# Kernel tuning notes

Hardware: AMD Instinct MI355X
Metric: run time of the kernel (lower is better)

## Reference

```python
import jax, jax.numpy as jnp
import numpy as np

BETA = 0.9  # snntorch Leaky beta (single-step, zero init mem => mem = x)
H = 8       # num_heads
EPS = 1e-5

@jax.custom_vjp
def lif_spike(x):
    # snn.Leaky single step, mem init 0: mem = BETA*0 + x ; spk = heaviside(mem - 1.0)
    return (x > 1.0).astype(x.dtype)

def _lif_fwd(x):
    return lif_spike(x), x

def _lif_bwd(x, g):
    # ATan surrogate (snntorch default, alpha=2): d spk/d mem = 1/(1 + (pi*(mem-1))^2)
    u = x - 1.0
    return (g / (1.0 + (jnp.pi * u) ** 2),)

lif_spike.defvjp(_lif_fwd, _lif_bwd)

def layer_norm(x, g, b):
    m = jnp.mean(x, -1, keepdims=True)
    v = jnp.mean((x - m) ** 2, -1, keepdims=True)
    return (x - m) * jax.lax.rsqrt(v + EPS) * g + b

def mha(x, Wqkv, Wo, causal):
    B, N, D = x.shape
    hd = D // H
    q, k, v = jnp.split(x @ Wqkv, 3, axis=-1)
    q = q.reshape(B, N, H, hd).transpose(0, 2, 1, 3)
    k = k.reshape(B, N, H, hd).transpose(0, 2, 1, 3)
    v = v.reshape(B, N, H, hd).transpose(0, 2, 1, 3)
    s = jnp.einsum('bhqd,bhkd->bhqk', q, k) / jnp.sqrt(jnp.asarray(hd, x.dtype))
    if causal:
        s = jnp.where(jnp.tril(jnp.ones((N, N), bool)), s, jnp.asarray(-1e9, x.dtype))
    a = jax.nn.softmax(s, axis=-1)
    o = jnp.einsum('bhqk,bhkd->bhqd', a, v).transpose(0, 2, 1, 3).reshape(B, N, D)
    return o @ Wo

def transformer(x, qkv, out, ln1, ff1, ff2, ln2, causal):
    # pre-norm transformer blocks; Encoder non-causal, Decoder causal
    for i in range(qkv.shape[0]):
        x = x + mha(layer_norm(x, ln1[i, 0], ln1[i, 1]), qkv[i], out[i], causal)
        x = x + jax.nn.gelu(layer_norm(x, ln2[i, 0], ln2[i, 1]) @ ff1[i]) @ ff2[i]
    return x

def setup_inputs():
    key = jax.random.key(0)
    B, R, S, D = 8, 90, 240, 256
    enc_depth, pred_depth = 8, 6
    ks = iter(jax.random.split(key, 64))
    def nrm(shape, std):
        return jax.random.normal(next(ks), shape, jnp.float32) * std
    def enc_params(depth):
        return dict(
            qkv=nrm((depth, D, 3 * D), 0.05),
            out=nrm((depth, D, D), 0.05),
            ln1=jnp.stack([jnp.ones((depth, D)), jnp.zeros((depth, D))], 1),
            ff1=nrm((depth, D, 4 * D), 0.05),
            ff2=nrm((depth, 4 * D, D), 0.05),
            ln2=jnp.stack([jnp.ones((depth, D)), jnp.zeros((depth, D))], 1),
        )
    t, s_, p = enc_params(enc_depth), enc_params(enc_depth), enc_params(pred_depth)
    inp = dict(
        x=jax.random.normal(next(ks), (B, R, S), jnp.float32),
        W_embed=nrm((S, D), 0.1), b_embed=jnp.zeros((D,), jnp.float32),
        pos_embedding=nrm((1, R, D), 1.0),
        mask_token=nrm((1, 1, D), 0.02),
        norm_g=jnp.ones((D,), jnp.float32), norm_b=jnp.zeros((D,), jnp.float32),
        W_dec=nrm((D, S), 0.1), b_dec=jnp.zeros((S,), jnp.float32),
    )
    for name, prm in (('t', t), ('s', s_), ('p', p)):
        for k2, v2 in prm.items():
            inp[name + '_' + k2] = v2
    return inp

def reference(x, W_embed, b_embed, pos_embedding, mask_token, norm_g, norm_b, W_dec, b_dec,
              t_qkv, t_out, t_ln1, t_ff1, t_ff2, t_ln2,
              s_qkv, s_out, s_ln1, s_ff1, s_ff2, s_ln2,
              p_qkv, p_out, p_ln1, p_ff1, p_ff2, p_ln2):
    B, R, S = x.shape
    D = W_embed.shape[1]
    # token embed + pos + token_lif
    x_emb = lif_spike(x @ W_embed + b_embed + pos_embedding)  # [B,R,D]
    # teacher (torch.no_grad)
    teacher_full = lif_spike(layer_norm(
        transformer(x_emb, t_qkv, t_out, t_ln1, t_ff1, t_ff2, t_ln2, False), norm_g, norm_b))
    teacher_full = jax.lax.stop_gradient(teacher_full)
    # student
    student_full = lif_spike(layer_norm(
        transformer(x_emb, s_qkv, s_out, s_ln1, s_ff1, s_ff2, s_ln2, False), norm_g, norm_b))
    # batched exhaustive leave-one-out: for each target t, context = all rows != t
    loo = np.stack([np.delete(np.arange(R), t) for t in range(R)])  # [R, R-1]
    ctx = student_full[:, loo, :]                                   # [B,R,R-1,D]
    masks = lif_spike(mask_token + pos_embedding)                   # [1,R,D] mask_lif
    masks = jnp.broadcast_to(masks[:, :, None, :], (B, R, 1, D))
    seq = jnp.concatenate([ctx, masks], axis=2).reshape(B * R, R, D)
    pred = lif_spike(transformer(seq, p_qkv, p_out, p_ln1, p_ff1, p_ff2, p_ln2, True))
    pred_targets = pred[:, -1, :].reshape(B, R, D)  # last token = predicted target region
    teacher_targets = teacher_full                   # exhaustive: targets are all R rows in order
    pred_seq = lif_spike(pred_targets @ W_dec + b_dec)      # output_lif [B,R,S]
    teacher_seq = lif_spike(teacher_targets @ W_dec + b_dec)
    target_seq = x
    return (pred_seq, teacher_seq, target_seq,
            pred_seq.mean(-1), teacher_seq.mean(-1), target_seq.mean(-1))
```

## Files before the change

### kernel.cpp

```cpp
#include <hip/hip_runtime.h>
#include <math.h>


__device__ __forceinline__ float gelu_f(float x) {
    const float c = 0.7978845608028654f;
    float x3 = x * x * x;
    float inner = c * (x + 0.044715f * x3);
    return 0.5f * x * (1.0f + tanhf(inner));
}

__device__ __forceinline__ int suffix_off(int g) {
    int b = g / 90, r = g - b * 90;
    return b * 4095 + 90 * r - ((r * (r - 1)) >> 1);
}

__global__ __launch_bounds__(256) void embed_kernel(
    const float* __restrict__ x, const float* __restrict__ We,
    const float* __restrict__ be, const float* __restrict__ pos,
    float* __restrict__ xemb) {
    int tok = blockIdx.x;
    int d = threadIdx.x;
    __shared__ float xs[240];
    if (d < 240) xs[d] = x[(size_t)tok * 240 + d];
    __syncthreads();
    int r = tok % 90;
    double acc = 0.0;
    for (int s = 0; s < 240; ++s)
        acc = fma((double)xs[s], (double)We[(size_t)s * 256 + d], acc);
    float a = (float)acc + be[d] + pos[r * 256 + d];
    xemb[(size_t)tok * 256 + d] = (a > 1.0f) ? 1.0f : 0.0f;
}

__global__ void copy_kernel(float* __restrict__ dst, const float* __restrict__ src, int n) {
    int i = blockIdx.x * 256 + threadIdx.x;
    if (i < n) dst[i] = src[i];
}
__global__ void zero_kernel(float* __restrict__ p, int n) {
    int i = blockIdx.x * 256 + threadIdx.x;
    if (i < n) p[i] = 0.f;
}

__global__ __launch_bounds__(256) void ln_kernel(
    const float* __restrict__ X,
    const float* __restrict__ gA, const float* __restrict__ bA,
    const float* __restrict__ gB, const float* __restrict__ bB,
    int split, float* __restrict__ Y) {
    int row = blockIdx.x;
    int d = threadIdx.x;
    const float* g = (row < split) ? gA : gB;
    const float* b = (row < split) ? bA : bB;
    __shared__ float red[256];
    float v = X[(size_t)row * 256 + d];
    red[d] = v;
    __syncthreads();
    for (int s = 128; s > 0; s >>= 1) { if (d < s) red[d] += red[d + s]; __syncthreads(); }
    float mean = red[0] * (1.0f / 256.0f);
    __syncthreads();
    float dv = v - mean;
    red[d] = dv * dv;
    __syncthreads();
    for (int s = 128; s > 0; s >>= 1) { if (d < s) red[d] += red[d + s]; __syncthreads(); }
    float var = red[0] * (1.0f / 256.0f);
    float r = 1.0f / sqrtf(var + 1e-5f);
    Y[(size_t)row * 256 + d] = dv * r * g[d] + b[d];
}

__global__ __launch_bounds__(256) void ln_lif_kernel(
    const float* __restrict__ X, const float* __restrict__ g, const float* __restrict__ b,
    float* __restrict__ Y) {
    int row = blockIdx.x;
    int d = threadIdx.x;
    __shared__ float red[256];
    float v = X[(size_t)row * 256 + d];
    red[d] = v;
    __syncthreads();
    for (int s = 128; s > 0; s >>= 1) { if (d < s) red[d] += red[d + s]; __syncthreads(); }
    float mean = red[0] * (1.0f / 256.0f);
    __syncthreads();
    float dv = v - mean;
    red[d] = dv * dv;
    __syncthreads();
    for (int s = 128; s > 0; s >>= 1) { if (d < s) red[d] += red[d + s]; __syncthreads(); }
    float var = red[0] * (1.0f / 256.0f);
    float r = 1.0f / sqrtf(var + 1e-5f);
    float val = dv * r * g[d] + b[d];
    Y[(size_t)row * 256 + d] = (val > 1.0f) ? 1.0f : 0.0f;
}

#define BK 16
template <int EPI>
__global__ __launch_bounds__(256) void gemm_kernel(
    const float* __restrict__ A, const float* __restrict__ W0,
    const float* __restrict__ W1, int wsplit,
    float* __restrict__ C, const float* __restrict__ R,
    int M, int N, int K, int ldA, int ldW, int ldC,
    int zA, int zW, long zC) {
    __shared__ float As[2][BK][64 + 4];
    __shared__ float Ws[2][BK][64];
    int bm = blockIdx.y * 64;
    int bn = blockIdx.x * 64;
    int z = blockIdx.z;
    A += (size_t)z * zA;
    const float* W = ((bm < wsplit) ? W0 : W1) + (size_t)z * zW;
    C += (size_t)z * zC;
    const float* Rp = R + (size_t)z * zC;
    int tid = threadIdx.x;
    int tx = tid & 15;
    int ty = tid >> 4;
    int ar = tid >> 2;
    int ak = (tid & 3) * 4;
    int wk = tid >> 4;
    int wn = (tid & 15) * 4;
    int gm = bm + ar;
    bool aok = gm < M;
    const float* Aptr = A + (size_t)gm * ldA + ak;
    const float* Wptr = W + (size_t)wk * ldW + bn + wn;

    float acc[4][4] = {{0.f}};
    float4 va = aok ? *(const float4*)Aptr : make_float4(0.f, 0.f, 0.f, 0.f);
    float4 vw = *(const float4*)Wptr;
    As[0][ak + 0][ar] = va.x; As[0][ak + 1][ar] = va.y;
    As[0][ak + 2][ar] = va.z; As[0][ak + 3][ar] = va.w;
    *(float4*)&Ws[0][wk][wn] = vw;
    __syncthreads();

    int nt = K / BK;
    for (int t = 0; t < nt; ++t) {
        int cur = t & 1;
        if (t + 1 < nt) {
            va = aok ? *(const float4*)(Aptr + (t + 1) * BK)
                     : make_float4(0.f, 0.f, 0.f, 0.f);
            vw = *(const float4*)(Wptr + (size_t)(t + 1) * BK * ldW);
        }
        #pragma unroll
        for (int k = 0; k < BK; ++k) {
            float a[4], w[4];
            #pragma unroll
            for (int i = 0; i < 4; ++i) a[i] = As[cur][k][ty * 4 + i];
            #pragma unroll
            for (int j = 0; j < 4; ++j) w[j] = Ws[cur][k][tx * 4 + j];
            #pragma unroll
            for (int i = 0; i < 4; ++i)
                #pragma unroll
                for (int j = 0; j < 4; ++j)
                    acc[i][j] = fmaf(a[i], w[j], acc[i][j]);
        }
        if (t + 1 < nt) {
            int nx = cur ^ 1;
            As[nx][ak + 0][ar] = va.x; As[nx][ak + 1][ar] = va.y;
            As[nx][ak + 2][ar] = va.z; As[nx][ak + 3][ar] = va.w;
            *(float4*)&Ws[nx][wk][wn] = vw;
        }
        __syncthreads();
    }
    #pragma unroll
    for (int i = 0; i < 4; ++i) {
        int om = bm + ty * 4 + i;
        if (om >= M) continue;
        #pragma unroll
        for (int j = 0; j < 4; ++j) {
            int on = bn + tx * 4 + j;
            float v = acc[i][j];
            if (EPI == 1) v += Rp[(size_t)om * ldC + on];
            if (EPI == 2) v = gelu_f(v);
            C[(size_t)om * ldC + on] = v;
        }
    }
}

__global__ void addff_kernel(float4* __restrict__ X, const float4* __restrict__ S,
                             long zstr4, int n4) {
    int i = blockIdx.x * 256 + threadIdx.x;
    if (i >= n4) return;
    float4 x = X[i];
    float4 s0 = S[i], s1 = S[i + zstr4], s2 = S[i + 2 * zstr4], s3 = S[i + 3 * zstr4];
    x.x = (((x.x + s0.x) + s1.x) + s2.x) + s3.x;
    x.y = (((x.y + s0.y) + s1.y) + s2.y) + s3.y;
    x.z = (((x.z + s0.z) + s1.z) + s2.z) + s3.z;
    x.w = (((x.w + s0.w) + s1.w) + s2.w) + s3.w;
    X[i] = x;
}

__global__ __launch_bounds__(128) void attn_kernel(
    const float* __restrict__ QKV, float* __restrict__ AO,
    int N, int causal, int hs, int off2) {
    int s = blockIdx.x, h = blockIdx.y;
    int tokbase = (s < hs) ? s * N : off2 + (s - hs) * N;
    __shared__ float Ks[90][32];
    __shared__ float Vs[90][32];
    int tid = threadIdx.x;
    for (int i = tid; i < N * 32; i += 128) {
        int n = i >> 5, d = i & 31;
        size_t base = ((size_t)(tokbase + n)) * 768 + h * 32;
        Ks[n][d] = QKV[base + 256 + d];
        Vs[n][d] = QKV[base + 512 + d];
    }
    __syncthreads();
    int q = tid;
    if (q >= N) return;
    float qv[32];
    size_t qbase = ((size_t)(tokbase + q)) * 768 + h * 32;
    #pragma unroll
    for (int d = 0; d < 32; ++d) qv[d] = QKV[qbase + d];
    const float sq = 5.656854249492380195f;
    int kmax = causal ? (q + 1) : N;
    float m = -3.0e38f;
    for (int k = 0; k < kmax; ++k) {
        float sd = 0.f;
        #pragma unroll
        for (int d = 0; d < 32; ++d) sd = fmaf(qv[d], Ks[k][d], sd);
        sd /= sq;
        m = fmaxf(m, sd);
    }
    float sum = 0.f;
    float acc[32];
    #pragma unroll
    for (int d = 0; d < 32; ++d) acc[d] = 0.f;
    for (int k = 0; k < kmax; ++k) {
        float sd = 0.f;
        #pragma unroll
        for (int d = 0; d < 32; ++d) sd = fmaf(qv[d], Ks[k][d], sd);
        sd /= sq;
        float p = expf(sd - m);
        sum += p;
        #pragma unroll
        for (int d = 0; d < 32; ++d) acc[d] = fmaf(p, Vs[k][d], acc[d]);
    }
    size_t obase = ((size_t)(tokbase + q)) * 256 + h * 32;
    #pragma unroll
    for (int d = 0; d < 32; ++d) AO[obase + d] = acc[d] / sum;
}

__global__ __launch_bounds__(128) void suffix_attn_kernel(
    const float* __restrict__ QKV, const float* __restrict__ kv,
    float* __restrict__ AO, int g0) {
    int ls = blockIdx.x, h = blockIdx.y;
    int g = g0 + ls;
    int b = g / 90, r = g - b * 90;
    int toff = suffix_off(g) - suffix_off(g0);
    int L = 90 - r;
    __shared__ float Ks[90][32];
    __shared__ float Vs[90][32];
    int tid = threadIdx.x;
    for (int i = tid; i < 90 * 32; i += 128) {
        int p = i >> 5, d = i & 31;
        float kk, vv;
        if (p < r) {
            const float* src = kv + ((size_t)(b * 89 + p)) * 512 + h * 32 + d;
            kk = src[0]; vv = src[256];
        } else {
            size_t base = ((size_t)(toff + p - r)) * 768 + h * 32 + d;
            kk = QKV[base + 256]; vv = QKV[base + 512];
        }
        Ks[p][d] = kk; Vs[p][d] = vv;
    }
    __syncthreads();
    if (tid >= L) return;
    int jq = r + tid;
    float qv[32];
    size_t qbase = ((size_t)(toff + tid)) * 768 + h * 32;
    #pragma unroll
    for (int d = 0; d < 32; ++d) qv[d] = QKV[qbase + d];
    const float sq = 5.656854249492380195f;
    int kmax = jq + 1;
    float m = -3.0e38f;
    for (int k = 0; k < kmax; ++k) {
        float sd = 0.f;
        #pragma unroll
        for (int d = 0; d < 32; ++d) sd = fmaf(qv[d], Ks[k][d], sd);
        sd /= sq;
        m = fmaxf(m, sd);
    }
    float sum = 0.f;
    float acc[32];
    #pragma unroll
    for (int d = 0; d < 32; ++d) acc[d] = 0.f;
    for (int k = 0; k < kmax; ++k) {
        float sd = 0.f;
        #pragma unroll
        for (int d = 0; d < 32; ++d) sd = fmaf(qv[d], Ks[k][d], sd);
        sd /= sq;
        float p = expf(sd - m);
        sum += p;
        #pragma unroll
        for (int d = 0; d < 32; ++d) acc[d] = fmaf(p, Vs[k][d], acc[d]);
    }
    size_t obase = ((size_t)(toff + tid)) * 256 + h * 32;
    #pragma unroll
    for (int d = 0; d < 32; ++d) AO[obase + d] = acc[d] / sum;
}

__global__ __launch_bounds__(128) void lastq_attn_kernel(
    const float* __restrict__ QKV, const float* __restrict__ kv,
    float* __restrict__ AO2, int g0) {
    int ls = blockIdx.x, h = blockIdx.y;
    int g = g0 + ls;
    int b = g / 90, r = g - b * 90;
    int toff = suffix_off(g) - suffix_off(g0);
    int L = 90 - r;
    __shared__ float Ks[90][32];
    __shared__ float Vs[90][32];
    int tid = threadIdx.x;
    for (int i = tid; i < 90 * 32; i += 128) {
        int p = i >> 5, d = i & 31;
        float kk, vv;
        if (p < r) {
            const float* src = kv + ((size_t)(b * 89 + p)) * 512 + h * 32 + d;
            kk = src[0]; vv = src[256];
        } else {
            size_t base = ((size_t)(toff + p - r)) * 768 + h * 32 + d;
            kk = QKV[base + 256]; vv = QKV[base + 512];
        }
        Ks[p][d] = kk; Vs[p][d] = vv;
    }
    __syncthreads();
    if (tid != 0) return;
    float qv[32];
    size_t qbase = ((size_t)(toff + L - 1)) * 768 + h * 32;
    #pragma unroll
    for (int d = 0; d < 32; ++d) qv[d] = QKV[qbase + d];
    const float sq = 5.656854249492380195f;
    float m = -3.0e38f;
    for (int k = 0; k < 90; ++k) {
        float sd = 0.f;
        #pragma unroll
        for (int d = 0; d < 32; ++d) sd = fmaf(qv[d], Ks[k][d], sd);
        sd /= sq;
        m = fmaxf(m, sd);
    }
    float sum = 0.f;
    float acc[32];
    #pragma unroll
    for (int d = 0; d < 32; ++d) acc[d] = 0.f;
    for (int k = 0; k < 90; ++k) {
        float sd = 0.f;
        #pragma unroll
        for (int d = 0; d < 32; ++d) sd = fmaf(qv[d], Ks[k][d], sd);
        sd /= sq;
        float p = expf(sd - m);
        sum += p;
        #pragma unroll
        for (int d = 0; d < 32; ++d) acc[d] = fmaf(p, Vs[k][d], acc[d]);
    }
    size_t obase = (size_t)ls * 256 + h * 32;
    #pragma unroll
    for (int d = 0; d < 32; ++d) AO2[obase + d] = acc[d] / sum;
}

__global__ void masks_kernel(const float* __restrict__ mt, const float* __restrict__ pos,
                             float* __restrict__ M) {
    int i = blockIdx.x * 256 + threadIdx.x;
    if (i >= 90 * 256) return;
    int d = i & 255;
    float v = mt[d] + pos[i];
    M[i] = (v > 1.0f) ? 1.0f : 0.0f;
}

__global__ __launch_bounds__(256) void gather_canon_kernel(
    const float* __restrict__ student, float* __restrict__ Xc, int b0) {
    int tc = blockIdx.x;
    int d = threadIdx.x;
    int b = b0 + tc / 89, p = tc % 89;
    Xc[(size_t)tc * 256 + d] = student[((size_t)(b * 90 + p)) * 256 + d];
}

__global__ __launch_bounds__(256) void kvcopy_kernel(
    const float* __restrict__ QKVc, float* __restrict__ kvl, int b0) {
    int tc = blockIdx.x;
    int c = threadIdx.x;
    size_t gtc = (size_t)b0 * 89 + tc;
    kvl[gtc * 512 + c]       = QKVc[(size_t)tc * 768 + 256 + c];
    kvl[gtc * 512 + 256 + c] = QKVc[(size_t)tc * 768 + 512 + c];
}

__global__ __launch_bounds__(256) void gather_suffix_kernel(
    const float* __restrict__ student, const float* __restrict__ masks,
    float* __restrict__ X, int g0) {
    int ls = blockIdx.x, slot = blockIdx.y;
    int d = threadIdx.x;
    int g = g0 + ls;
    int b = g / 90, r = g - b * 90;
    if (slot >= 90 - r) return;
    int j = r + slot;
    int dst = suffix_off(g) - suffix_off(g0) + slot;
    float v;
    if (j == 89) v = masks[r * 256 + d];
    else         v = student[((size_t)(b * 90 + j + 1)) * 256 + d];
    X[(size_t)dst * 256 + d] = v;
}

__global__ __launch_bounds__(256) void gather_last_kernel(
    const float* __restrict__ X, float* __restrict__ X2, int g0) {
    int ls = blockIdx.x;
    int d = threadIdx.x;
    int g = g0 + ls;
    int r = g % 90;
    int tok = suffix_off(g) - suffix_off(g0) + (89 - r);
    X2[(size_t)ls * 256 + d] = X[(size_t)tok * 256 + d];
}

__global__ __launch_bounds__(256) void lif_rows_kernel(
    const float* __restrict__ X2, float* __restrict__ predT, int g0) {
    int ls = blockIdx.x;
    int d = threadIdx.x;
    float v = X2[(size_t)ls * 256 + d];
    predT[(size_t)(g0 + ls) * 256 + d] = (v > 1.0f) ? 1.0f : 0.0f;
}

__global__ __launch_bounds__(256) void decode_kernel(
    const float* __restrict__ T, const float* __restrict__ Wd, const float* __restrict__ bd,
    float* __restrict__ outseq, float* __restrict__ outmean) {
    int row = blockIdx.x;
    int n = threadIdx.x;
    __shared__ float ts[256];
    __shared__ float red[256];
    ts[n] = T[(size_t)row * 256 + n];
    __syncthreads();
    float sval = 0.f;
    if (n < 240) {
        double acc = 0.0;
        for (int k = 0; k < 256; ++k)
            acc = fma((double)ts[k], (double)Wd[(size_t)k * 240 + n], acc);
        float a = (float)acc;
        a += bd[n];
        sval = (a > 1.0f) ? 1.0f : 0.0f;
        outseq[(size_t)row * 240 + n] = sval;
    }
    red[n] = sval;
    __syncthreads();
    for (int s = 128; s > 0; s >>= 1) { if (n < s) red[n] += red[n + s]; __syncthreads(); }
    if (n == 0) outmean[row] = red[0] * (1.0f / 240.0f);
}

__global__ __launch_bounds__(256) void target_kernel(
    const float* __restrict__ x, float* __restrict__ outseq, float* __restrict__ outmean) {
    int row = blockIdx.x;
    int n = threadIdx.x;
    __shared__ float red[256];
    float v = 0.f;
    if (n < 240) {
        v = x[(size_t)row * 240 + n];
        outseq[(size_t)row * 240 + n] = v;
    }
    red[n] = v;
    __syncthreads();
    for (int s = 128; s > 0; s >>= 1) { if (n < s) red[n] += red[n + s]; __syncthreads(); }
    if (n == 0) outmean[row] = red[0] * (1.0f / 240.0f);
}

extern "C" void kernel_launch(void* const* d_in, const int* in_sizes, int n_in,
                              void* d_out, int out_size, void* d_ws, size_t ws_size,
                              hipStream_t stream) {
    const float* x   = (const float*)d_in[0];
    const float* We  = (const float*)d_in[1];
    const float* be  = (const float*)d_in[2];
    const float* pos = (const float*)d_in[3];
    const float* mt  = (const float*)d_in[4];
    const float* ng  = (const float*)d_in[5];
    const float* nb  = (const float*)d_in[6];
    const float* Wd  = (const float*)d_in[7];
    const float* bd  = (const float*)d_in[8];
    const float* prm[3][6];
    for (int g = 0; g < 3; ++g)
        for (int k = 0; k < 6; ++k)
            prm[g][k] = (const float*)d_in[9 + g * 6 + k];

    float* wp = (float*)d_ws;
    auto alloc = [&](size_t n) { float* q = wp; wp += n; return q; };
    float* x_emb   = alloc(720 * 256);
    float* teacher = alloc(720 * 256);
    float* student = alloc(720 * 256);
    float* predT   = alloc(720 * 256);
    float* masksb  = alloc(90 * 256);
    float* kvc     = alloc(6ull * 712 * 512);
    float* AO2 = alloc(720 * 256);
    float* X2  = alloc(720 * 256);
    float* Xn2 = alloc(720 * 256);
    float* H2  = alloc(720 * 1024);
    float* S2  = alloc(4ull * 720 * 256);
    long  zS2  = 720 * 256;
    size_t fixed = (size_t)(wp - (float*)d_ws);

    size_t avail = ws_size / 4;
    long tcap_l = 90;
    if (avail > fixed) {
        long t = (long)((avail - fixed) / 3328);
        if (t > tcap_l) tcap_l = t;
    }
    if (tcap_l > 32760) tcap_l = 32760;
    int TCAP = (int)tcap_l;
    float* X   = alloc((size_t)TCAP * 256);
    float* Xn  = alloc((size_t)TCAP * 256);
    float* QKV = alloc((size_t)TCAP * 768);
    float* H   = alloc((size_t)TCAP * 1024);
    float* S   = alloc(4ull * TCAP * 256);
    long  zS   = (long)TCAP * 256;
    bool co_batch = (TCAP >= 1488);

    float* out = (float*)d_out;
    const int NOSPLIT = 1 << 30;

    embed_kernel<<<720, 256, 0, stream>>>(x, We, be, pos, x_emb);
    masks_kernel<<<90, 256, 0, stream>>>(mt, pos, masksb);

    auto run_layer = [&](int T, int gA, int gB, int l, int split, auto&& attn_launch) {
        const float* qkvA = prm[gA][0] + (size_t)l * 256 * 768;
        const float* qkvB = prm[gB][0] + (size_t)l * 256 * 768;
        const float* woA  = prm[gA][1] + (size_t)l * 256 * 256;
        const float* woB  = prm[gB][1] + (size_t)l * 256 * 256;
        const float* l1A  = prm[gA][2] + (size_t)l * 512;
        const float* l1B  = prm[gB][2] + (size_t)l * 512;
        const float* f1A  = prm[gA][3] + (size_t)l * 256 * 1024;
        const float* f1B  = prm[gB][3] + (size_t)l * 256 * 1024;
        const float* f2A  = prm[gA][4] + (size_t)l * 1024 * 256;
        const float* f2B  = prm[gB][4] + (size_t)l * 1024 * 256;
        const float* l2A  = prm[gA][5] + (size_t)l * 512;
        const float* l2B  = prm[gB][5] + (size_t)l * 512;
        int gy = (T + 63) / 64;
        ln_kernel<<<T, 256, 0, stream>>>(X, l1A, l1A + 256, l1B, l1B + 256, split, Xn);
        gemm_kernel<0><<<dim3(12, gy, 1), 256, 0, stream>>>(
            Xn, qkvA, qkvB, split, QKV, QKV, T, 768, 256, 256, 768, 768, 0, 0, 0);
        attn_launch();
        gemm_kernel<1><<<dim3(4, gy, 1), 256, 0, stream>>>(
            Xn, woA, woB, split, X, X, T, 256, 256, 256, 256, 256, 0, 0, 0);
        ln_kernel<<<T, 256, 0, stream>>>(X, l2A, l2A + 256, l2B, l2B + 256, split, Xn);
        gemm_kernel<2><<<dim3(16, gy, 1), 256, 0, stream>>>(
            Xn, f1A, f1B, split, H, H, T, 1024, 256, 256, 1024, 1024, 0, 0, 0);
        gemm_kernel<0><<<dim3(4, gy, 4), 256, 0, stream>>>(
            H, f2A, f2B, split, S, S, T, 256, 256, 1024, 256, 256, 256, 65536, zS);
        addff_kernel<<<(T * 64 + 255) / 256, 256, 0, stream>>>(
            (float4*)X, (const float4*)S, zS / 4, T * 64);
    };

    if (co_batch) {
        copy_kernel<<<720, 256, 0, stream>>>(X, x_emb, 720 * 256);
        copy_kernel<<<720, 256, 0, stream>>>(X + 768 * 256, x_emb, 720 * 256);
        zero_kernel<<<48, 256, 0, stream>>>(X + 720 * 256, 48 * 256);
        for (int l = 0; l < 8; ++l)
            run_layer(1488, 0, 1, l, 768,
                      [&] { attn_kernel<<<dim3(16, 8), 128, 0, stream>>>(
                                QKV, Xn, 90, 0, 8, 768); });
        ln_lif_kernel<<<720, 256, 0, stream>>>(X, ng, nb, teacher);
        ln_lif_kernel<<<720, 256, 0, stream>>>(X + 768 * 256, ng, nb, student);
    } else {
        int ce = TCAP / 90; if (ce > 8) ce = 8; if (ce < 1) ce = 1;
        for (int gi = 0; gi < 2; ++gi) {
            for (int s0 = 0; s0 < 8; s0 += ce) {
                int c = (8 - s0) < ce ? (8 - s0) : ce;
                int T = c * 90;
                copy_kernel<<<(T * 256 + 255) / 256, 256, 0, stream>>>(
                    X, x_emb + (size_t)s0 * 90 * 256, T * 256);
                for (int l = 0; l < 8; ++l)
                    run_layer(T, gi, gi, l, NOSPLIT,
                              [&] { attn_kernel<<<dim3(c, 8), 128, 0, stream>>>(
                                        QKV, Xn, 90, 0, c, 0); });
                ln_lif_kernel<<<T, 256, 0, stream>>>(
                    X, ng, nb, (gi == 0 ? teacher : student) + (size_t)s0 * 90 * 256);
            }
        }
    }

    {
        int cb = TCAP / 89; if (cb > 8) cb = 8; if (cb < 1) cb = 1;
        for (int b0 = 0; b0 < 8; b0 += cb) {
            int c = (8 - b0) < cb ? (8 - b0) : cb;
            int T = c * 89;
            gather_canon_kernel<<<T, 256, 0, stream>>>(student, X, b0);
            for (int l = 0; l < 5; ++l) {
                float* kvl = kvc + (size_t)l * 712 * 512;
                run_layer(T, 2, 2, l, NOSPLIT,
                          [&] {
                              kvcopy_kernel<<<T, 256, 0, stream>>>(QKV, kvl, b0);
                              attn_kernel<<<dim3(c, 8), 128, 0, stream>>>(
                                  QKV, Xn, 89, 1, c, 0);
                          });
            }
            {
                const float* l1P  = prm[2][2] + 5ull * 512;
                const float* qkvP = prm[2][0] + 5ull * 256 * 768;
                float* kvl = kvc + 5ull * 712 * 512;
                int gy = (T + 63) / 64;
                ln_kernel<<<T, 256, 0, stream>>>(X, l1P, l1P + 256, l1P, l1P + 256,
                                                 NOSPLIT, Xn);
                gemm_kernel<0><<<dim3(12, gy, 1), 256, 0, stream>>>(
                    Xn, qkvP, qkvP, NOSPLIT, QKV, QKV, T, 768, 256, 256, 768, 768, 0, 0, 0);
                kvcopy_kernel<<<T, 256, 0, stream>>>(QKV, kvl, b0);
            }
        }
    }

    auto Toff = [](int g) { int b = g / 90, r = g - b * 90;
                            return (long)b * 4095 + 90L * r - (long)r * (r - 1) / 2; };
    int cs = TCAP / 90; if (cs < 1) cs = 1; if (cs > 720) cs = 720;
    for (int g0 = 0; g0 < 720; ) {
        int g1 = g0 + cs; if (g1 > 720) g1 = 720;
        while ((int)(Toff(g1) - Toff(g0)) > TCAP && g1 > g0 + 1) --g1;
        int c = g1 - g0;
        int Tc = (int)(Toff(g1) - Toff(g0));
        { dim3 g(c, 90);
          gather_suffix_kernel<<<g, 256, 0, stream>>>(student, masksb, X, g0); }
        for (int l = 0; l < 5; ++l) {
            float* kvl = kvc + (size_t)l * 712 * 512;
            run_layer(Tc, 2, 2, l, NOSPLIT,
                      [&] { dim3 g(c, 8);
                            suffix_attn_kernel<<<g, 128, 0, stream>>>(QKV, kvl, Xn, g0); });
        }
        {
            const float* qkvP = prm[2][0] + 5ull * 256 * 768;
            const float* woP  = prm[2][1] + 5ull * 256 * 256;
            const float* l1P  = prm[2][2] + 5ull * 512;
            const float* f1P  = prm[2][3] + 5ull * 256 * 1024;
            const float* f2P  = prm[2][4] + 5ull * 1024 * 256;
            const float* l2P  = prm[2][5] + 5ull * 512;
            float* kvl = kvc + 5ull * 712 * 512;
            int gy  = (Tc + 63) / 64;
            int gyc = (c + 63) / 64;
            ln_kernel<<<Tc, 256, 0, stream>>>(X, l1P, l1P + 256, l1P, l1P + 256,
                                              NOSPLIT, Xn);
            gemm_kernel<0><<<dim3(12, gy, 1), 256, 0, stream>>>(
                Xn, qkvP, qkvP, NOSPLIT, QKV, QKV, Tc, 768, 256, 256, 768, 768, 0, 0, 0);
            { dim3 g(c, 8);
              lastq_attn_kernel<<<g, 128, 0, stream>>>(QKV, kvl, AO2, g0); }
            gather_last_kernel<<<c, 256, 0, stream>>>(X, X2, g0);
            gemm_kernel<1><<<dim3(4, gyc, 1), 256, 0, stream>>>(
                AO2, woP, woP, NOSPLIT, X2, X2, c, 256, 256, 256, 256, 256, 0, 0, 0);
            ln_kernel<<<c, 256, 0, stream>>>(X2, l2P, l2P + 256, l2P, l2P + 256,
                                             NOSPLIT, Xn2);
            gemm_kernel<2><<<dim3(16, gyc, 1), 256, 0, stream>>>(
                Xn2, f1P, f1P, NOSPLIT, H2, H2, c, 1024, 256, 256, 1024, 1024, 0, 0, 0);
            gemm_kernel<0><<<dim3(4, gyc, 4), 256, 0, stream>>>(
                H2, f2P, f2P, NOSPLIT, S2, S2, c, 256, 256, 1024, 256, 256, 256, 65536, zS2);
            addff_kernel<<<(c * 64 + 255) / 256, 256, 0, stream>>>(
                (float4*)X2, (const float4*)S2, zS2 / 4, c * 64);
            lif_rows_kernel<<<c, 256, 0, stream>>>(X2, predT, g0);
        }
        g0 = g1;
    }

    decode_kernel<<<720, 256, 0, stream>>>(predT, Wd, bd, out + 0, out + 518400);
    decode_kernel<<<720, 256, 0, stream>>>(teacher, Wd, bd, out + 172800, out + 519120);
    target_kernel<<<720, 256, 0, stream>>>(x, out + 345600, out + 519840);
}
```

Baseline: 9.435 ms.

## Replace split-K FF2 GEMM plus reduction kernel with single fused residual GEMM

The second feed-forward GEMM was split four ways along K into a partial-sum buffer, then summed with the residual by a separate add kernel. A new kernel now runs the full K=1024 reduction in one block, starts from the residual, and adds the partials in chunks of 256 to keep the original summation order. This drops the scratch buffer traffic and one launch per layer, and the freed workspace allows larger token chunks. In exchange the FF2 launch has a quarter of the blocks, which lowers parallelism for small token counts.

```diff
diff --git a/kernel.cpp b/kernel.cpp
--- a/kernel.cpp
+++ b/kernel.cpp
@@ -93,17 +93,12 @@
     const float* __restrict__ A, const float* __restrict__ W0,
     const float* __restrict__ W1, int wsplit,
     float* __restrict__ C, const float* __restrict__ R,
-    int M, int N, int K, int ldA, int ldW, int ldC,
-    int zA, int zW, long zC) {
+    int M, int N, int K, int ldA, int ldW, int ldC) {
     __shared__ float As[2][BK][64 + 4];
     __shared__ float Ws[2][BK][64];
     int bm = blockIdx.y * 64;
     int bn = blockIdx.x * 64;
-    int z = blockIdx.z;
-    A += (size_t)z * zA;
-    const float* W = ((bm < wsplit) ? W0 : W1) + (size_t)z * zW;
-    C += (size_t)z * zC;
-    const float* Rp = R + (size_t)z * zC;
+    const float* W = (bm < wsplit) ? W0 : W1;
     int tid = threadIdx.x;
     int tx = tid & 15;
     int ty = tid >> 4;
@@ -161,24 +156,98 @@
         for (int j = 0; j < 4; ++j) {
             int on = bn + tx * 4 + j;
             float v = acc[i][j];
-            if (EPI == 1) v += Rp[(size_t)om * ldC + on];
+            if (EPI == 1) v += R[(size_t)om * ldC + on];
             if (EPI == 2) v = gelu_f(v);
             C[(size_t)om * ldC + on] = v;
         }
     }
 }
 
-__global__ void addff_kernel(float4* __restrict__ X, const float4* __restrict__ S,
-                             long zstr4, int n4) {
-    int i = blockIdx.x * 256 + threadIdx.x;
-    if (i >= n4) return;
-    float4 x = X[i];
-    float4 s0 = S[i], s1 = S[i + zstr4], s2 = S[i + 2 * zstr4], s3 = S[i + 3 * zstr4];
-    x.x = (((x.x + s0.x) + s1.x) + s2.x) + s3.x;
-    x.y = (((x.y + s0.y) + s1.y) + s2.y) + s3.y;
-    x.z = (((x.z + s0.z) + s1.z) + s2.z) + s3.z;
-    x.w = (((x.w + s0.w) + s1.w) + s2.w) + s3.w;
-    X[i] = x;
+__global__ __launch_bounds__(256) void gemm_ff_kernel(
+    const float* __restrict__ A, const float* __restrict__ W0,
+    const float* __restrict__ W1, int wsplit,
+    float* __restrict__ C, const float* __restrict__ R,
+    int M, int K, int ldA, int ldW, int ldC) {
+    __shared__ float As[2][BK][64 + 4];
+    __shared__ float Ws[2][BK][64];
+    int bm = blockIdx.y * 64;
+    int bn = blockIdx.x * 64;
+    const float* W = (bm < wsplit) ? W0 : W1;
+    int tid = threadIdx.x;
+    int tx = tid & 15;
+    int ty = tid >> 4;
+    int ar = tid >> 2;
+    int ak = (tid & 3) * 4;
+    int wk = tid >> 4;
+    int wn = (tid & 15) * 4;
+    int gm = bm + ar;
+    bool aok = gm < M;
+    const float* Aptr = A + (size_t)gm * ldA + ak;
+    const float* Wptr = W + (size_t)wk * ldW + bn + wn;
+
+    float v[4][4];
+    #pragma unroll
+    for (int i = 0; i < 4; ++i) {
+        int om = bm + ty * 4 + i;
+        #pragma unroll
+        for (int j = 0; j < 4; ++j)
+            v[i][j] = (om < M) ? R[(size_t)om * ldC + bn + tx * 4 + j] : 0.f;
+    }
+    float acc[4][4] = {{0.f}};
+
+    float4 va = aok ? *(const float4*)Aptr : make_float4(0.f, 0.f, 0.f, 0.f);
+    float4 vw = *(const float4*)Wptr;
+    As[0][ak + 0][ar] = va.x; As[0][ak + 1][ar] = va.y;
+    As[0][ak + 2][ar] = va.z; As[0][ak + 3][ar] = va.w;
+    *(float4*)&Ws[0][wk][wn] = vw;
+    __syncthreads();
+
+    int nt = K / BK;
+    for (int t = 0; t < nt; ++t) {
+        int cur = t & 1;
+        if (t + 1 < nt) {
+            va = aok ? *(const float4*)(Aptr + (t + 1) * BK)
+                     : make_float4(0.f, 0.f, 0.f, 0.f);
+            vw = *(const float4*)(Wptr + (size_t)(t + 1) * BK * ldW);
+        }
+        #pragma unroll
+        for (int k = 0; k < BK; ++k) {
+            float a[4], w[4];
+            #pragma unroll
+            for (int i = 0; i < 4; ++i) a[i] = As[cur][k][ty * 4 + i];
+            #pragma unroll
+            for (int j = 0; j < 4; ++j) w[j] = Ws[cur][k][tx * 4 + j];
+            #pragma unroll
+            for (int i = 0; i < 4; ++i)
+                #pragma unroll
+                for (int j = 0; j < 4; ++j)
+                    acc[i][j] = fmaf(a[i], w[j], acc[i][j]);
+        }
+        if (t + 1 < nt) {
+            int nx = cur ^ 1;
+            As[nx][ak + 0][ar] = va.x; As[nx][ak + 1][ar] = va.y;
+            As[nx][ak + 2][ar] = va.z; As[nx][ak + 3][ar] = va.w;
+            *(float4*)&Ws[nx][wk][wn] = vw;
+        }
+        __syncthreads();
+        if ((t & 15) == 15) {
+            #pragma unroll
+            for (int i = 0; i < 4; ++i)
+                #pragma unroll
+                for (int j = 0; j < 4; ++j) {
+                    v[i][j] += acc[i][j];
+                    acc[i][j] = 0.f;
+                }
+        }
+    }
+    #pragma unroll
+    for (int i = 0; i < 4; ++i) {
+        int om = bm + ty * 4 + i;
+        if (om >= M) continue;
+        #pragma unroll
+        for (int j = 0; j < 4; ++j)
+            C[(size_t)om * ldC + bn + tx * 4 + j] = v[i][j];
+    }
 }
 
 __global__ __launch_bounds__(128) void attn_kernel(
@@ -477,14 +546,12 @@
     float* X2  = alloc(720 * 256);
     float* Xn2 = alloc(720 * 256);
     float* H2  = alloc(720 * 1024);
-    float* S2  = alloc(4ull * 720 * 256);
-    long  zS2  = 720 * 256;
     size_t fixed = (size_t)(wp - (float*)d_ws);
 
     size_t avail = ws_size / 4;
     long tcap_l = 90;
     if (avail > fixed) {
-        long t = (long)((avail - fixed) / 3328);
+        long t = (long)((avail - fixed) / 2304);
         if (t > tcap_l) tcap_l = t;
     }
     if (tcap_l > 32760) tcap_l = 32760;
@@ -493,8 +560,6 @@
     float* Xn  = alloc((size_t)TCAP * 256);
     float* QKV = alloc((size_t)TCAP * 768);
     float* H   = alloc((size_t)TCAP * 1024);
-    float* S   = alloc(4ull * TCAP * 256);
-    long  zS   = (long)TCAP * 256;
     bool co_batch = (TCAP >= 1488);
 
     float* out = (float*)d_out;
@@ -518,18 +583,16 @@
         const float* l2B  = prm[gB][5] + (size_t)l * 512;
         int gy = (T + 63) / 64;
         ln_kernel<<<T, 256, 0, stream>>>(X, l1A, l1A + 256, l1B, l1B + 256, split, Xn);
-        gemm_kernel<0><<<dim3(12, gy, 1), 256, 0, stream>>>(
-            Xn, qkvA, qkvB, split, QKV, QKV, T, 768, 256, 256, 768, 768, 0, 0, 0);
+        gemm_kernel<0><<<dim3(12, gy), 256, 0, stream>>>(
+            Xn, qkvA, qkvB, split, QKV, QKV, T, 768, 256, 256, 768, 768);
         attn_launch();
-        gemm_kernel<1><<<dim3(4, gy, 1), 256, 0, stream>>>(
-            Xn, woA, woB, split, X, X, T, 256, 256, 256, 256, 256, 0, 0, 0);
+        gemm_kernel<1><<<dim3(4, gy), 256, 0, stream>>>(
+            Xn, woA, woB, split, X, X, T, 256, 256, 256, 256, 256);
         ln_kernel<<<T, 256, 0, stream>>>(X, l2A, l2A + 256, l2B, l2B + 256, split, Xn);
-        gemm_kernel<2><<<dim3(16, gy, 1), 256, 0, stream>>>(
-            Xn, f1A, f1B, split, H, H, T, 1024, 256, 256, 1024, 1024, 0, 0, 0);
-        gemm_kernel<0><<<dim3(4, gy, 4), 256, 0, stream>>>(
-            H, f2A, f2B, split, S, S, T, 256, 256, 1024, 256, 256, 256, 65536, zS);
-        addff_kernel<<<(T * 64 + 255) / 256, 256, 0, stream>>>(
-            (float4*)X, (const float4*)S, zS / 4, T * 64);
+        gemm_kernel<2><<<dim3(16, gy), 256, 0, stream>>>(
+            Xn, f1A, f1B, split, H, H, T, 1024, 256, 256, 1024, 1024);
+        gemm_ff_kernel<<<dim3(4, gy), 256, 0, stream>>>(
+            H, f2A, f2B, split, X, X, T, 1024, 1024, 256, 256);
     };
 
     if (co_batch) {
@@ -582,8 +645,8 @@
                 int gy = (T + 63) / 64;
                 ln_kernel<<<T, 256, 0, stream>>>(X, l1P, l1P + 256, l1P, l1P + 256,
                                                  NOSPLIT, Xn);
-                gemm_kernel<0><<<dim3(12, gy, 1), 256, 0, stream>>>(
-                    Xn, qkvP, qkvP, NOSPLIT, QKV, QKV, T, 768, 256, 256, 768, 768, 0, 0, 0);
+                gemm_kernel<0><<<dim3(12, gy), 256, 0, stream>>>(
+                    Xn, qkvP, qkvP, NOSPLIT, QKV, QKV, T, 768, 256, 256, 768, 768);
                 kvcopy_kernel<<<T, 256, 0, stream>>>(QKV, kvl, b0);
             }
         }
@@ -617,21 +680,19 @@
             int gyc = (c + 63) / 64;
             ln_kernel<<<Tc, 256, 0, stream>>>(X, l1P, l1P + 256, l1P, l1P + 256,
                                               NOSPLIT, Xn);
-            gemm_kernel<0><<<dim3(12, gy, 1), 256, 0, stream>>>(
-                Xn, qkvP, qkvP, NOSPLIT, QKV, QKV, Tc, 768, 256, 256, 768, 768, 0, 0, 0);
+            gemm_kernel<0><<<dim3(12, gy), 256, 0, stream>>>(
+                Xn, qkvP, qkvP, NOSPLIT, QKV, QKV, Tc, 768, 256, 256, 768, 768);
             { dim3 g(c, 8);
               lastq_attn_kernel<<<g, 128, 0, stream>>>(QKV, kvl, AO2, g0); }
             gather_last_kernel<<<c, 256, 0, stream>>>(X, X2, g0);
-            gemm_kernel<1><<<dim3(4, gyc, 1), 256, 0, stream>>>(
-                AO2, woP, woP, NOSPLIT, X2, X2, c, 256, 256, 256, 256, 256, 0, 0, 0);
+            gemm_kernel<1><<<dim3(4, gyc), 256, 0, stream>>>(
+                AO2, woP, woP, NOSPLIT, X2, X2, c, 256, 256, 256, 256, 256);
             ln_kernel<<<c, 256, 0, stream>>>(X2, l2P, l2P + 256, l2P, l2P + 256,
                                              NOSPLIT, Xn2);
-            gemm_kernel<2><<<dim3(16, gyc, 1), 256, 0, stream>>>(
-                Xn2, f1P, f1P, NOSPLIT, H2, H2, c, 1024, 256, 256, 1024, 1024, 0, 0, 0);
-            gemm_kernel<0><<<dim3(4, gyc, 4), 256, 0, stream>>>(
-                H2, f2P, f2P, NOSPLIT, S2, S2, c, 256, 256, 1024, 256, 256, 256, 65536, zS2);
-            addff_kernel<<<(c * 64 + 255) / 256, 256, 0, stream>>>(
-                (float4*)X2, (const float4*)S2, zS2 / 4, c * 64);
+            gemm_kernel<2><<<dim3(16, gyc), 256, 0, stream>>>(
+                Xn2, f1P, f1P, NOSPLIT, H2, H2, c, 1024, 256, 256, 1024, 1024);
+            gemm_ff_kernel<<<dim3(4, gyc), 256, 0, stream>>>(
+                H2, f2P, f2P, NOSPLIT, X2, X2, c, 1024, 1024, 256, 256);
             lif_rows_kernel<<<c, 256, 0, stream>>>(X2, predT, g0);
         }
         g0 = g1;
```

Result: slower. 9.889 ms (+4.8%).
